# Optimization experiments

Hardware: AMD Instinct MI355X
Metric: run time of the kernel (lower is better)

Reference implementation:

```python
import jax, jax.numpy as jnp
import numpy as np
from jax import lax

B, C_IN, IMG, P, HID = 128, 3, 224, 16, 768
HW = (IMG // P) ** 2  # 196 patches


def setup_inputs() -> dict:
    key = jax.random.key(0)
    k1, k2, k3, k4 = jax.random.split(key, 4)
    x = jax.random.normal(k1, (B, C_IN, IMG, IMG), dtype=jnp.float32)
    # conv weight init scale ~ kaiming-ish, value irrelevant for correctness
    W = jax.random.normal(k2, (HID, C_IN, P, P), dtype=jnp.float32) * 0.02
    b = jax.random.normal(k3, (HID,), dtype=jnp.float32) * 0.02
    # per-sample random permutation of patch positions (the pixel shuffle)
    perm = jax.vmap(lambda k: jax.random.permutation(k, HW))(jax.random.split(k4, B)).astype(jnp.int32)
    return {"x": x, "W": W, "b": b, "perm": perm}


def reference(x, W, b, perm):
    # patchify conv: kernel_size == stride == P, no padding
    enc = lax.conv_general_dilated(
        x, W, window_strides=(P, P), padding="VALID",
        dimension_numbers=("NCHW", "OIHW", "NCHW"),
    ) + b[None, :, None, None]                      # [B, HID, H', W']
    Bc, Cc, Hc, Wc = enc.shape
    enc = enc.reshape(Bc, Cc, Hc * Wc).transpose(0, 2, 1)   # [B, HW, HID]
    # per-sample patch shuffle: shuffled[i, j] = enc[i, perm[i, j]]
    shuffled = jnp.take_along_axis(enc, perm[:, :, None], axis=1)
    return shuffled
```

## Files before the change

kernel.cpp:

```cpp
#include <hip/hip_runtime.h>
#include <hip/hip_bf16.h>

#define BATCH  128
#define HWN    196
#define HIDN   768
#define KN     768
#define IMGSZ  224
#define IMG2   (224*224)
#define MTOT   (BATCH*HWN)

#define BM 128
#define BN 128
#define BK 32

typedef __attribute__((ext_vector_type(8))) short bf16x8;
typedef __attribute__((ext_vector_type(4))) float floatx4;

#define GP(p) ((const __attribute__((address_space(1))) void*)(p))
#define SP(p) ((__attribute__((address_space(3))) void*)(p))

static __device__ __forceinline__ short f2bf(float f) {
    __hip_bfloat16 h = __float2bfloat16(f);
    return __builtin_bit_cast(short, h);
}

static __device__ __forceinline__ bf16x8 cvt8(const float* __restrict__ src) {
    float4 f0 = *(const float4*)(src);
    float4 f1 = *(const float4*)(src + 4);
    bf16x8 v;
    v[0]=f2bf(f0.x); v[1]=f2bf(f0.y); v[2]=f2bf(f0.z); v[3]=f2bf(f0.w);
    v[4]=f2bf(f1.x); v[5]=f2bf(f1.y); v[6]=f2bf(f1.z); v[7]=f2bf(f1.w);
    return v;
}

__global__ __launch_bounds__(256)
void prep_A(const float* __restrict__ x, const int* __restrict__ perm,
            unsigned short* __restrict__ A)
{
    const int idx = blockIdx.x * 256 + threadIdx.x;
    const int gr  = idx / 48;
    const int seg = idx - gr * 48;
    const int b   = gr / HWN;
    const int p   = perm[gr];
    const int py  = p / 14, px = p - py * 14;
    const int c   = seg >> 4;
    const int iy  = seg & 15;

    const float* src = x + (size_t)b * 3 * IMG2 + (size_t)c * IMG2
                         + (size_t)(py * 16 + iy) * IMGSZ + px * 16;
    bf16x8 v0 = cvt8(src);
    bf16x8 v1 = cvt8(src + 8);
    unsigned short* dst = A + (size_t)gr * KN + seg * 16;
    *(bf16x8*)(dst)     = v0;
    *(bf16x8*)(dst + 8) = v1;
}

__global__ __launch_bounds__(256)
void prep_W(const float* __restrict__ W, unsigned short* __restrict__ Wb)
{
    const int idx = blockIdx.x * 256 + threadIdx.x;
    const float* src = W + (size_t)idx * 8;
    *(bf16x8*)(Wb + (size_t)idx * 8) = cvt8(src);
}

__global__ __launch_bounds__(256, 3)
void gemm(const unsigned short* __restrict__ A, const unsigned short* __restrict__ Wb,
          const float* __restrict__ bias, float* __restrict__ out)
{
    __shared__ __align__(16) unsigned short As[BM * BK];
    __shared__ __align__(16) unsigned short Bs[BN * BK];

    const int tid = threadIdx.x;
    const int bm  = blockIdx.x;
    const int bn  = blockIdx.y;

    const int srow = tid >> 2;
    const int sseg = tid & 3;
    const unsigned short* ga = A  + (size_t)(bm * BM + srow) * KN + sseg * 8;
    const unsigned short* gb = Wb + (size_t)(bn * BN + srow) * KN + sseg * 8;

    const int lane = tid & 63;
    const int wave = tid >> 6;
    const int wm = (wave >> 1) * 64;
    const int wn = (wave & 1) * 64;
    const int lr = lane & 15;
    const int lq = lane >> 4;

    floatx4 acc[4][4] = {};

    for (int k0 = 0; k0 < KN; k0 += BK) {
        __builtin_amdgcn_global_load_lds(GP(ga + k0),            SP(&As[tid * 8]),        16, 0, 0);
        __builtin_amdgcn_global_load_lds(GP(ga + 64 * KN + k0),  SP(&As[2048 + tid * 8]), 16, 0, 0);
        __builtin_amdgcn_global_load_lds(GP(gb + k0),            SP(&Bs[tid * 8]),        16, 0, 0);
        __builtin_amdgcn_global_load_lds(GP(gb + 64 * KN + k0),  SP(&Bs[2048 + tid * 8]), 16, 0, 0);
        __syncthreads();

        bf16x8 bfrag[4];
        #pragma unroll
        for (int j = 0; j < 4; ++j)
            bfrag[j] = *(const bf16x8*)&Bs[(wn + j * 16 + lr) * BK + lq * 8];
        #pragma unroll
        for (int i = 0; i < 4; ++i) {
            bf16x8 afrag = *(const bf16x8*)&As[(wm + i * 16 + lr) * BK + lq * 8];
            #pragma unroll
            for (int j = 0; j < 4; ++j)
                acc[i][j] = __builtin_amdgcn_mfma_f32_16x16x32_bf16(
                                afrag, bfrag[j], acc[i][j], 0, 0, 0);
        }
        __syncthreads();
    }

    #pragma unroll
    for (int j = 0; j < 4; ++j) {
        const int gc = bn * BN + wn + j * 16 + lr;
        const float bv = bias[gc];
        #pragma unroll
        for (int i = 0; i < 4; ++i) {
            const int grow = bm * BM + wm + i * 16 + lq * 4;
            float* op = out + (size_t)grow * HIDN + gc;
            #pragma unroll
            for (int r = 0; r < 4; ++r)
                op[(size_t)r * HIDN] = acc[i][j][r] + bv;
        }
    }
}

extern "C" void kernel_launch(void* const* d_in, const int* in_sizes, int n_in,
                              void* d_out, int out_size, void* d_ws, size_t ws_size,
                              hipStream_t stream) {
    const float* x    = (const float*)d_in[0];
    const float* W    = (const float*)d_in[1];
    const float* bias = (const float*)d_in[2];
    const int*   perm = (const int*)d_in[3];
    float* out = (float*)d_out;

    unsigned short* A  = (unsigned short*)d_ws;
    unsigned short* Wb = A + (size_t)MTOT * KN;

    prep_A<<<dim3(MTOT * 48 / 256), dim3(256), 0, stream>>>(x, perm, A);
    prep_W<<<dim3(KN * HIDN / 8 / 256), dim3(256), 0, stream>>>(W, Wb);
    gemm<<<dim3(MTOT / BM, HIDN / BN), dim3(256), 0, stream>>>(A, Wb, bias, out);
}
```

Baseline: 192.3 us.

## Double-buffer GEMM LDS tiles, swap MFMA operands for vector stores, reorder grid

```diff
diff --git a/kernel.cpp b/kernel.cpp
--- a/kernel.cpp
+++ b/kernel.cpp
@@ -63,16 +63,16 @@
     *(bf16x8*)(Wb + (size_t)idx * 8) = cvt8(src);
 }
 
-__global__ __launch_bounds__(256, 3)
+__global__ __launch_bounds__(256, 4)
 void gemm(const unsigned short* __restrict__ A, const unsigned short* __restrict__ Wb,
           const float* __restrict__ bias, float* __restrict__ out)
 {
-    __shared__ __align__(16) unsigned short As[BM * BK];
-    __shared__ __align__(16) unsigned short Bs[BN * BK];
+    __shared__ __align__(16) unsigned short As[2][BM * BK];
+    __shared__ __align__(16) unsigned short Bs[2][BN * BK];
 
     const int tid = threadIdx.x;
-    const int bm  = blockIdx.x;
-    const int bn  = blockIdx.y;
+    const int bn  = blockIdx.x;
+    const int bm  = blockIdx.y;
 
     const int srow = tid >> 2;
     const int sseg = tid & 3;
@@ -88,39 +88,50 @@
 
     floatx4 acc[4][4] = {};
 
-    for (int k0 = 0; k0 < KN; k0 += BK) {
-        __builtin_amdgcn_global_load_lds(GP(ga + k0),            SP(&As[tid * 8]),        16, 0, 0);
-        __builtin_amdgcn_global_load_lds(GP(ga + 64 * KN + k0),  SP(&As[2048 + tid * 8]), 16, 0, 0);
-        __builtin_amdgcn_global_load_lds(GP(gb + k0),            SP(&Bs[tid * 8]),        16, 0, 0);
-        __builtin_amdgcn_global_load_lds(GP(gb + 64 * KN + k0),  SP(&Bs[2048 + tid * 8]), 16, 0, 0);
-        __syncthreads();
-
+    auto issue = [&](int k0, int b) {
+        __builtin_amdgcn_global_load_lds(GP(ga + k0),           SP(&As[b][tid * 8]),        16, 0, 0);
+        __builtin_amdgcn_global_load_lds(GP(ga + 64 * KN + k0), SP(&As[b][2048 + tid * 8]), 16, 0, 0);
+        __builtin_amdgcn_global_load_lds(GP(gb + k0),           SP(&Bs[b][tid * 8]),        16, 0, 0);
+        __builtin_amdgcn_global_load_lds(GP(gb + 64 * KN + k0), SP(&Bs[b][2048 + tid * 8]), 16, 0, 0);
+    };
+    auto compute = [&](int b) {
         bf16x8 bfrag[4];
         #pragma unroll
         for (int j = 0; j < 4; ++j)
-            bfrag[j] = *(const bf16x8*)&Bs[(wn + j * 16 + lr) * BK + lq * 8];
+            bfrag[j] = *(const bf16x8*)&Bs[b][(wn + j * 16 + lr) * BK + lq * 8];
         #pragma unroll
         for (int i = 0; i < 4; ++i) {
-            bf16x8 afrag = *(const bf16x8*)&As[(wm + i * 16 + lr) * BK + lq * 8];
+            bf16x8 afrag = *(const bf16x8*)&As[b][(wm + i * 16 + lr) * BK + lq * 8];
             #pragma unroll
             for (int j = 0; j < 4; ++j)
                 acc[i][j] = __builtin_amdgcn_mfma_f32_16x16x32_bf16(
-                                afrag, bfrag[j], acc[i][j], 0, 0, 0);
+                                bfrag[j], afrag, acc[i][j], 0, 0, 0);
         }
+    };
+
+    issue(0, 0);
+    for (int k0 = 0; k0 < KN; k0 += 2 * BK) {
         __syncthreads();
+        if (k0 + BK < KN) issue(k0 + BK, 1);
+        compute(0);
+        __syncthreads();
+        if (k0 + 2 * BK < KN) issue(k0 + 2 * BK, 0);
+        compute(1);
     }
 
     #pragma unroll
     for (int j = 0; j < 4; ++j) {
-        const int gc = bn * BN + wn + j * 16 + lr;
-        const float bv = bias[gc];
+        const int gc0 = bn * BN + wn + j * 16 + lq * 4;
+        const float4 bv = *(const float4*)&bias[gc0];
         #pragma unroll
         for (int i = 0; i < 4; ++i) {
-            const int grow = bm * BM + wm + i * 16 + lq * 4;
-            float* op = out + (size_t)grow * HIDN + gc;
-            #pragma unroll
-            for (int r = 0; r < 4; ++r)
-                op[(size_t)r * HIDN] = acc[i][j][r] + bv;
+            const int grow = bm * BM + wm + i * 16 + lr;
+            float4 v;
+            v.x = acc[i][j][0] + bv.x;
+            v.y = acc[i][j][1] + bv.y;
+            v.z = acc[i][j][2] + bv.z;
+            v.w = acc[i][j][3] + bv.w;
+            *(float4*)(out + (size_t)grow * HIDN + gc0) = v;
         }
     }
 }
@@ -139,5 +150,5 @@
 
     prep_A<<<dim3(MTOT * 48 / 256), dim3(256), 0, stream>>>(x, perm, A);
     prep_W<<<dim3(KN * HIDN / 8 / 256), dim3(256), 0, stream>>>(W, Wb);
-    gemm<<<dim3(MTOT / BM, HIDN / BN), dim3(256), 0, stream>>>(A, Wb, bias, out);
+    gemm<<<dim3(HIDN / BN, MTOT / BM), dim3(256), 0, stream>>>(A, Wb, bias, out);
 }
```

Result: slower. 197.4 us (+2.6%).
